# Performance work log

Measured on AMD Instinct MI355X. Metric: run time of the kernel, lower is better.

## Reference

```python
import jax, jax.numpy as jnp
import numpy as np

D_MODEL = 1024
NUM_HEADS = 16
SEQ_LEN = 2048
HEAD_DIM = D_MODEL // NUM_HEADS


def _rope_thetas(seq_len, head_dim):
    # Standard RoPE angles: theta[s, j] = s * 10000^(-2j/d), j in [0, d/2)
    d_half = head_dim // 2
    pos = jnp.arange(seq_len, dtype=jnp.float32)
    freqs = 1.0 / jnp.power(10000.0, jnp.arange(0, head_dim, 2, dtype=jnp.float32) / head_dim)
    thetas = pos[:, None] * freqs[None, :]  # [S, d_half]
    return jnp.cos(thetas), jnp.sin(thetas)


def _apply_rope(x, cos, sin):
    # x: [B, H, S, D]; rotate consecutive pairs (x_{2i}, x_{2i+1}) by theta_i
    b, h, s, d = x.shape
    xp = x.reshape(b, h, s, d // 2, 2)
    x1, x2 = xp[..., 0], xp[..., 1]
    c = cos[None, None, :, :]
    sn = sin[None, None, :, :]
    o1 = x1 * c - x2 * sn
    o2 = x1 * sn + x2 * c
    return jnp.stack([o1, o2], axis=-1).reshape(b, h, s, d)


def setup_inputs() -> dict:
    key = jax.random.key(0)
    k_x, k_wqkv, k_bqkv, k_wo, k_bo = jax.random.split(key, 5)
    lim_qkv = 1.0 / np.sqrt(D_MODEL)
    x = jax.random.normal(k_x, (2, SEQ_LEN, D_MODEL), dtype=jnp.float32)
    w_qkv = jax.random.uniform(k_wqkv, (3 * D_MODEL, D_MODEL), jnp.float32, -lim_qkv, lim_qkv)
    b_qkv = jax.random.uniform(k_bqkv, (3 * D_MODEL,), jnp.float32, -lim_qkv, lim_qkv)
    w_out = jax.random.uniform(k_wo, (D_MODEL, D_MODEL), jnp.float32, -lim_qkv, lim_qkv)
    b_out = jax.random.uniform(k_bo, (D_MODEL,), jnp.float32, -lim_qkv, lim_qkv)
    return {"x": x, "w_qkv": w_qkv, "b_qkv": b_qkv, "w_out": w_out, "b_out": b_out}


def reference(x, w_qkv, b_qkv, w_out, b_out):
    B, S, D = x.shape
    H, Dh = NUM_HEADS, D // NUM_HEADS
    qkv = x @ w_qkv.T + b_qkv  # [B, S, 3D]
    q, k, v = jnp.split(qkv, 3, axis=-1)
    # [B, S, D] -> [B, H, S, Dh]
    q = q.reshape(B, S, H, Dh).transpose(0, 2, 1, 3)
    k = k.reshape(B, S, H, Dh).transpose(0, 2, 1, 3)
    v = v.reshape(B, S, H, Dh).transpose(0, 2, 1, 3)
    cos, sin = _rope_thetas(S, Dh)
    q = _apply_rope(q, cos, sin)
    k = _apply_rope(k, cos, sin)
    scores = jnp.einsum('bhqd,bhkd->bhqk', q, k) / jnp.sqrt(jnp.float32(Dh))
    causal = jnp.tril(jnp.ones((S, S), dtype=bool))
    scores = jnp.where(causal[None, None, :, :], scores, jnp.float32(-jnp.inf))
    attn = jax.nn.softmax(scores, axis=-1)
    o = jnp.einsum('bhqk,bhkd->bhqd', attn, v)  # [B, H, S, Dh]
    o = o.transpose(0, 2, 1, 3).reshape(B, S, D)
    return o @ w_out.T + b_out
```

## Files before the change

### kernel.cpp

```cpp
#include <hip/hip_runtime.h>
#include <stdint.h>

#define S_LEN 2048
#define NH 16
#define DM 1024
#define HD 64
#define NB 2
#define TOK (NB * S_LEN)

typedef __attribute__((ext_vector_type(8))) short short8v;
typedef __attribute__((ext_vector_type(4))) float f32x4;
typedef __attribute__((ext_vector_type(2))) unsigned int u32x2;
typedef unsigned short u16;
typedef unsigned int u32;

__device__ __forceinline__ float bf2f(u16 u) {
    u32 x = ((u32)u) << 16;
    return __builtin_bit_cast(float, x);
}
__device__ __forceinline__ u16 f2bf(float f) {
    u32 u = __builtin_bit_cast(u32, f);
    return (u16)((u + 0x7FFFu + ((u >> 16) & 1u)) >> 16);
}
__device__ __forceinline__ u32 cvtpk(float lo, float hi) {
    u32 r;
    asm("v_cvt_pk_bf16_f32 %0, %1, %2" : "=v"(r) : "v"(lo), "v"(hi));
    return r;
}

__device__ __forceinline__ void gld_lds16(const void* g, void* lds_base_uniform) {
    auto gp = (const __attribute__((address_space(1))) u32*)(uintptr_t)g;
    auto lp = (__attribute__((address_space(3))) u32*)(uintptr_t)(u32)(uintptr_t)lds_base_uniform;
    __builtin_amdgcn_global_load_lds(gp, lp, 16, 0, 0);
}

__global__ void detect_dtype(const u32* __restrict__ xw, int* __restrict__ flag) {
    __shared__ int cnt[4];
    const int t = threadIdx.x;
    int c = 0;
#pragma unroll
    for (int j = 0; j < 16; ++j) {
        const u32 wd = xw[(t * 16 + j) * 64];
        const u32 e = (wd >> 7) & 0xFF;
        c += (e >= 0x58 && e <= 0x98) ? 1 : 0;
    }
#pragma unroll
    for (int off = 1; off < 64; off <<= 1) c += __shfl_xor(c, off);
    if ((t & 63) == 0) cnt[t >> 6] = c;
    __syncthreads();
    if (t == 0) flag[0] = (cnt[0] + cnt[1] + cnt[2] + cnt[3] >= 2600) ? 1 : 0;
}

#define XCH (TOK * DM / 8)
#define WQCH (3 * DM * DM / 8)
#define WOCH (DM * DM / 8)
#define CONVTOT (XCH + WQCH + WOCH)
#define TABN (S_LEN * 16)
__global__ __launch_bounds__(256) void convert_all(
    const void* __restrict__ xs, const void* __restrict__ wqs, const void* __restrict__ wos,
    u16* __restrict__ xd, u16* __restrict__ wqd, u16* __restrict__ wod,
    float* __restrict__ tab, const int* __restrict__ flagp) {
    int i = blockIdx.x * 256 + threadIdx.x;
    if (i >= CONVTOT) {
        const int e = i - CONVTOT;
        const int s = e & 2047;
        const int i2 = e >> 11;
        const float fa = expf(-(float)(2 * i2) * 0.2878231366242557f);
        const float fb = expf(-(float)(2 * i2 + 1) * 0.2878231366242557f);
        float sa, ca, sb, cb;
        sincosf((float)s * fa, &sa, &ca);
        sincosf((float)s * fb, &sb, &cb);
        f32x4 tv = {ca, sa, cb, sb};
        *(f32x4*)(tab + (size_t)e * 4) = tv;
        return;
    }
    const void* src;
    u16* dst;
    if (i < XCH) {
        src = xs; dst = xd;
    } else if (i < XCH + WQCH) {
        src = wqs; dst = wqd; i -= XCH;
    } else {
        src = wos; dst = wod; i -= XCH + WQCH;
    }
    if (flagp[0]) {
        ((short8v*)dst)[i] = ((const short8v*)src)[i];
    } else {
        const f32x4 v0 = ((const f32x4*)src)[2 * i];
        const f32x4 v1 = ((const f32x4*)src)[2 * i + 1];
        short8v o;
#pragma unroll
        for (int q = 0; q < 4; ++q) o[q] = (short)f2bf(v0[q]);
#pragma unroll
        for (int q = 0; q < 4; ++q) o[4 + q] = (short)f2bf(v1[q]);
        ((short8v*)dst)[i] = o;
    }
}

template <int MODE>
__global__ __launch_bounds__(256) void gemm_k(
    const u16* __restrict__ A, const u16* __restrict__ Bt,
    const void* __restrict__ biasv, void* __restrict__ Cv,
    int M, int N, int K, const int* __restrict__ flagp, int out_flagged,
    u16* __restrict__ qws, u16* __restrict__ kws,
    u16* __restrict__ vT, const float* __restrict__ tab) {
    __shared__ __align__(16) u16 lA[3][128 * 32];
    __shared__ __align__(16) u16 lB[3][128 * 32];
    const int fl = flagp[0];
    const int fo = out_flagged ? fl : 1;

    const int tid = threadIdx.x;
    const int w = __builtin_amdgcn_readfirstlane(tid >> 6);
    const int lane = tid & 63;
    const int quad = lane >> 4;
    const int l16 = lane & 15;
    const int bm = blockIdx.y * 128;
    const int bn = (MODE == 2 ? 2048 : 0) + blockIdx.x * 128;
    const int wm = (w >> 1) * 64;
    const int wn = (w & 1) * 64;

    f32x4 acc[4][4];
#pragma unroll
    for (int i = 0; i < 4; ++i)
#pragma unroll
        for (int j = 0; j < 4; ++j) acc[i][j] = {0.f, 0.f, 0.f, 0.f};

    const int kiters = K >> 5;
#define GEMM_STAGE(kk, buf)                                                            \
    {                                                                                  \
        _Pragma("unroll") for (int c = 0; c < 2; ++c) {                                \
            const int chunk = w * 2 + c;                                               \
            const int off = chunk * 1024 + lane * 16;                                  \
            const int m_ = off >> 6;                                                   \
            const int kb_ = off & 63;                                                  \
            gld_lds16((const char*)(A + (size_t)(bm + m_) * K + (kk) * 32) + kb_,      \
                      (char*)&lA[buf][0] + chunk * 1024);                              \
            gld_lds16((const char*)(Bt + (size_t)(bn + m_) * K + (kk) * 32) + kb_,     \
                      (char*)&lB[buf][0] + chunk * 1024);                              \
        }                                                                              \
    }

    GEMM_STAGE(0, 0);
    if (kiters > 1) GEMM_STAGE(1, 1);
    int cur = 0;
    for (int kk = 0; kk < kiters; ++kk) {
        if (kk + 1 < kiters) {
            asm volatile("s_waitcnt vmcnt(4)" ::: "memory");
        } else {
            asm volatile("s_waitcnt vmcnt(0)" ::: "memory");
        }
        __builtin_amdgcn_s_barrier();
        if (kk + 2 < kiters) {
            const int nb = (cur + 2 >= 3) ? cur - 1 : cur + 2;
            GEMM_STAGE(kk + 2, nb);
        }

        short8v af[4], bf[4];
#pragma unroll
        for (int t = 0; t < 4; ++t) {
            af[t] = *(const short8v*)&lA[cur][(wm + t * 16 + l16) * 32 + quad * 8];
            bf[t] = *(const short8v*)&lB[cur][(wn + t * 16 + l16) * 32 + quad * 8];
        }
        __builtin_amdgcn_s_setprio(1);
        if constexpr (MODE == 2) {
#pragma unroll
            for (int i = 0; i < 4; ++i)
#pragma unroll
                for (int j = 0; j < 4; ++j)
                    acc[i][j] =
                        __builtin_amdgcn_mfma_f32_16x16x32_bf16(af[i], bf[j], acc[i][j], 0, 0, 0);
        } else {
#pragma unroll
            for (int i = 0; i < 4; ++i)
#pragma unroll
                for (int j = 0; j < 4; ++j)
                    acc[i][j] =
                        __builtin_amdgcn_mfma_f32_16x16x32_bf16(bf[j], af[i], acc[i][j], 0, 0, 0);
        }
        __builtin_amdgcn_s_setprio(0);
        cur = (cur == 2) ? 0 : cur + 1;
    }
#undef GEMM_STAGE

    if constexpr (MODE == 0) {
#pragma unroll
        for (int j = 0; j < 4; ++j) {
            const int n0 = bn + wn + j * 16 + quad * 4;
            float bv0, bv1, bv2, bv3;
            if (fl) {
                const u32x2 bw = *(const u32x2*)((const u16*)biasv + n0);
                bv0 = bf2f((u16)(bw.x & 0xffff));
                bv1 = bf2f((u16)(bw.x >> 16));
                bv2 = bf2f((u16)(bw.y & 0xffff));
                bv3 = bf2f((u16)(bw.y >> 16));
            } else {
                const f32x4 bw = *(const f32x4*)((const float*)biasv + n0);
                bv0 = bw[0]; bv1 = bw[1]; bv2 = bw[2]; bv3 = bw[3];
            }
#pragma unroll
            for (int i = 0; i < 4; ++i) {
                const size_t base = (size_t)(bm + wm + i * 16 + l16) * N + n0;
                const float v0 = acc[i][j][0] + bv0, v1 = acc[i][j][1] + bv1;
                const float v2 = acc[i][j][2] + bv2, v3 = acc[i][j][3] + bv3;
                if (fo) {
                    u32x2 ov;
                    ov.x = cvtpk(v0, v1);
                    ov.y = cvtpk(v2, v3);
                    *(u32x2*)((u16*)Cv + base) = ov;
                } else {
                    f32x4 ov = {v0, v1, v2, v3};
                    *(f32x4*)((float*)Cv + base) = ov;
                }
            }
        }
    } else if constexpr (MODE == 2) {
#pragma unroll
        for (int j = 0; j < 4; ++j) {
            const int n = bn + wn + j * 16 + l16;
            const float bv = fl ? bf2f(((const u16*)biasv)[n]) : ((const float*)biasv)[n];
            const int vcol = n - 2048;
            const int hh = vcol >> 6, d = vcol & 63;
#pragma unroll
            for (int i = 0; i < 4; ++i) {
                const int m0 = bm + wm + i * 16 + quad * 4;
                const int bb = m0 >> 11, s0 = m0 & 2047;
                u32x2 ov;
                ov.x = cvtpk(acc[i][j][0] + bv, acc[i][j][1] + bv);
                ov.y = cvtpk(acc[i][j][2] + bv, acc[i][j][3] + bv);
                *(u32x2*)(vT + ((size_t)((bb * NH + hh) * HD + d)) * S_LEN + s0) = ov;
            }
        }
    } else {
        const bool isq = (blockIdx.x < 8);
        u16* outp = isq ? qws : kws;
#pragma unroll
        for (int j = 0; j < 4; ++j) {
            const int n0 = bn + wn + j * 16 + quad * 4;
            float bv0, bv1, bv2, bv3;
            if (fl) {
                const u32x2 bw = *(const u32x2*)((const u16*)biasv + n0);
                bv0 = bf2f((u16)(bw.x & 0xffff));
                bv1 = bf2f((u16)(bw.x >> 16));
                bv2 = bf2f((u16)(bw.y & 0xffff));
                bv3 = bf2f((u16)(bw.y >> 16));
            } else {
                const f32x4 bw = *(const f32x4*)((const float*)biasv + n0);
                bv0 = bw[0]; bv1 = bw[1]; bv2 = bw[2]; bv3 = bw[3];
            }
            const int nc = n0 & 1023;
            const int hh = nc >> 6;
            const int d0 = nc & 63;
            const int i2u = d0 >> 2;
#pragma unroll
            for (int i = 0; i < 4; ++i) {
                const int m = bm + wm + i * 16 + l16;
                const int bb = m >> 11, s = m & 2047;
                const f32x4 cs4 = *(const f32x4*)(tab + ((size_t)i2u * S_LEN + s) * 4);
                const float v0 = acc[i][j][0] + bv0, v1 = acc[i][j][1] + bv1;
                const float v2 = acc[i][j][2] + bv2, v3 = acc[i][j][3] + bv3;
                const float o0 = v0 * cs4[0] - v1 * cs4[1];
                const float o1 = v0 * cs4[1] + v1 * cs4[0];
                const float o2 = v2 * cs4[2] - v3 * cs4[3];
                const float o3 = v2 * cs4[3] + v3 * cs4[2];
                u32x2 ov;
                ov.x = cvtpk(o0, o1);
                ov.y = cvtpk(o2, o3);
                *(u32x2*)(outp + ((size_t)((bb * NH + hh) * S_LEN + s)) * HD + d0) = ov;
            }
        }
    }
}

__global__ __launch_bounds__(256, 3) void attn_kernel(
    const u16* __restrict__ qws, const u16* __restrict__ kws,
    const u16* __restrict__ vT, u16* __restrict__ ows) {
    __shared__ __align__(16) u16 kl[3][64 * 64];
    __shared__ __align__(16) u16 vl[2][64 * 64];
    __shared__ __align__(16) u32 pl32[4][16 * 36];
    const int t = threadIdx.x;
    const int w = __builtin_amdgcn_readfirstlane(t >> 6);
    const int lane = t & 63;
    const int quad = lane >> 4;
    const int l16 = lane & 15;

    const int id = blockIdx.x;
    const int g = id & 31;
    const int qb = 31 - (id >> 5);
    const int h = g & 15, b = g >> 4;
    const int q0 = qb * 64 + w * 16;

    const size_t bh = (size_t)(b * NH + h);
    const u16* qbp = qws + bh * (size_t)S_LEN * HD;
    const u16* kb = kws + bh * (size_t)S_LEN * HD;
    const u16* vb = vT + bh * (size_t)HD * S_LEN;

    const int r0 = lane >> 3;
    const int srcc = (lane & 7) ^ r0;
    const int xorb = (l16 & 7) << 4;

    short8v qf[2];
#pragma unroll
    for (int hf = 0; hf < 2; ++hf)
        qf[hf] = *(const short8v*)(qbp + (size_t)(q0 + l16) * HD + hf * 32 + quad * 8);

    f32x4 oaccT[4];
#pragma unroll
    for (int d = 0; d < 4; ++d) oaccT[d] = {0.f, 0.f, 0.f, 0.f};
    float mrow = -__builtin_inff();
    float lrow = 0.f;

#define STAGE_K(kt, buf)                                                            \
    {                                                                               \
        _Pragma("unroll") for (int s = 0; s < 2; ++s) {                             \
            const int row = w * 8 + s * 32 + r0;                                    \
            gld_lds16(kb + (size_t)((kt) * 64 + row) * HD + srcc * 8,               \
                      (char*)&kl[buf][0] + w * 1024 + s * 4096);                    \
        }                                                                           \
    }
#define STAGE_V(kt, buf)                                                            \
    {                                                                               \
        _Pragma("unroll") for (int s = 0; s < 2; ++s) {                             \
            const int row = w * 8 + s * 32 + r0;                                    \
            gld_lds16(vb + (size_t)row * S_LEN + (kt) * 64 + srcc * 8,              \
                      (char*)&vl[buf][0] + w * 1024 + s * 4096);                    \
        }                                                                           \
    }

    STAGE_K(0, 0);
    STAGE_V(0, 0);
    if (qb >= 1) STAGE_K(1, 1);

    int ck = 0;
    for (int kt = 0; kt <= qb; ++kt) {
        if (kt < qb) {
            asm volatile("s_waitcnt vmcnt(2)" ::: "memory");
        } else {
            asm volatile("s_waitcnt vmcnt(0)" ::: "memory");
        }
        __builtin_amdgcn_s_barrier();
        asm volatile("" ::: "memory");
        if (kt < qb) STAGE_V(kt + 1, (kt + 1) & 1);
        if (kt + 2 <= qb) {
            const int kn = (ck + 2 >= 3) ? ck - 1 : ck + 2;
            STAGE_K(kt + 2, kn);
        }
        const char* Kb = (const char*)&kl[ck][0];
        const char* Vb = (const char*)&vl[kt & 1][0];

        f32x4 s4[4];
        __builtin_amdgcn_s_setprio(1);
#pragma unroll
        for (int sub = 0; sub < 4; ++sub) {
            const int lin = (sub * 16 + l16) * 128 + quad * 16;
            const short8v k0 = *(const short8v*)(Kb + (lin ^ xorb));
            const short8v k1 = *(const short8v*)(Kb + ((lin + 64) ^ xorb));
            f32x4 a = {0.f, 0.f, 0.f, 0.f};
            a = __builtin_amdgcn_mfma_f32_16x16x32_bf16(k0, qf[0], a, 0, 0, 0);
            a = __builtin_amdgcn_mfma_f32_16x16x32_bf16(k1, qf[1], a, 0, 0, 0);
            s4[sub] = a;
        }
        __builtin_amdgcn_s_setprio(0);
        float sv[16];
#pragma unroll
        for (int sub = 0; sub < 4; ++sub)
#pragma unroll
            for (int r = 0; r < 4; ++r) sv[sub * 4 + r] = s4[sub][r] * 0.125f;
        if (kt == qb) {
            const int qloc = w * 16 + l16;
#pragma unroll
            for (int sub = 0; sub < 4; ++sub)
#pragma unroll
                for (int r = 0; r < 4; ++r)
                    if (sub * 16 + quad * 4 + r > qloc) sv[sub * 4 + r] = -__builtin_inff();
        }
        float a0 = fmaxf(sv[0], sv[1]), a1 = fmaxf(sv[2], sv[3]);
        float a2 = fmaxf(sv[4], sv[5]), a3 = fmaxf(sv[6], sv[7]);
        float a4 = fmaxf(sv[8], sv[9]), a5 = fmaxf(sv[10], sv[11]);
        float a6 = fmaxf(sv[12], sv[13]), a7 = fmaxf(sv[14], sv[15]);
        a0 = fmaxf(a0, a1); a2 = fmaxf(a2, a3);
        a4 = fmaxf(a4, a5); a6 = fmaxf(a6, a7);
        a0 = fmaxf(a0, a2); a4 = fmaxf(a4, a6);
        float mx = fmaxf(a0, a4);
        mx = fmaxf(mx, __shfl_xor(mx, 16));
        mx = fmaxf(mx, __shfl_xor(mx, 32));
        const float mnew = fmaxf(mrow, mx);
        const float alpha = __expf(mrow - mnew);
        mrow = mnew;
        float p[16];
#pragma unroll
        for (int i = 0; i < 16; ++i) p[i] = __expf(sv[i] - mnew);
        float b0 = p[0] + p[1], b1 = p[2] + p[3], b2 = p[4] + p[5], b3 = p[6] + p[7];
        float b4 = p[8] + p[9], b5 = p[10] + p[11], b6 = p[12] + p[13], b7 = p[14] + p[15];
        b0 += b1; b2 += b3; b4 += b5; b6 += b7;
        b0 += b2; b4 += b6;
        float ps = b0 + b4;
        ps += __shfl_xor(ps, 16);
        ps += __shfl_xor(ps, 32);
        lrow = lrow * alpha + ps;
#pragma unroll
        for (int d = 0; d < 4; ++d) oaccT[d] *= alpha;
        u32* prow = &pl32[w][l16 * 36];
#pragma unroll
        for (int sub = 0; sub < 4; ++sub) {
            u32x2 pw;
            pw.x = cvtpk(p[sub * 4 + 0], p[sub * 4 + 1]);
            pw.y = cvtpk(p[sub * 4 + 2], p[sub * 4 + 3]);
            *(u32x2*)&prow[sub * 8 + quad * 2] = pw;
        }
        asm volatile("s_waitcnt lgkmcnt(0)" ::: "memory");
        __builtin_amdgcn_sched_barrier(0);
        __builtin_amdgcn_s_setprio(1);
#pragma unroll
        for (int c2 = 0; c2 < 2; ++c2) {
            const short8v pf = *(const short8v*)&pl32[w][l16 * 36 + c2 * 16 + quad * 4];
#pragma unroll
            for (int d = 0; d < 4; ++d) {
                const int lin = (d * 16 + l16) * 128 + c2 * 64 + quad * 16;
                const short8v vfd = *(const short8v*)(Vb + (lin ^ xorb));
                oaccT[d] = __builtin_amdgcn_mfma_f32_16x16x32_bf16(vfd, pf, oaccT[d], 0, 0, 0);
            }
        }
        __builtin_amdgcn_s_setprio(0);
        ck = (ck == 2) ? 0 : ck + 1;
    }
#undef STAGE_K
#undef STAGE_V

    const float inv = 1.0f / lrow;
    const size_t rowbase = ((size_t)(b * S_LEN + q0 + l16)) * DM + h * HD;
#pragma unroll
    for (int df = 0; df < 4; ++df) {
        const int d0 = df * 16 + quad * 4;
        u32x2 ov;
        ov.x = cvtpk(oaccT[df][0] * inv, oaccT[df][1] * inv);
        ov.y = cvtpk(oaccT[df][2] * inv, oaccT[df][3] * inv);
        *(u32x2*)(ows + rowbase + d0) = ov;
    }
}

extern "C" void kernel_launch(void* const* d_in, const int* in_sizes, int n_in,
                              void* d_out, int out_size, void* d_ws, size_t ws_size,
                              hipStream_t stream) {
    const void* x = d_in[0];
    const void* w_qkv = d_in[1];
    const void* b_qkv = d_in[2];
    const void* w_out = d_in[3];
    const void* b_out = d_in[4];

    int* flag = (int*)d_ws;
    u16* xb = (u16*)d_ws + 8;
    u16* wqkvb = xb + (size_t)TOK * DM;
    u16* woutb = wqkvb + (size_t)3 * DM * DM;
    u16* qws = woutb + (size_t)DM * DM;
    u16* kws = qws + (size_t)NB * NH * S_LEN * HD;
    u16* vT = kws + (size_t)NB * NH * S_LEN * HD;
    u16* ows = vT + (size_t)NB * NH * HD * S_LEN;
    float* tab = (float*)(ows + (size_t)TOK * DM);

    detect_dtype<<<1, 256, 0, stream>>>((const u32*)x, flag);
    convert_all<<<(CONVTOT + TABN) / 256, 256, 0, stream>>>(
        x, w_qkv, w_out, xb, wqkvb, woutb, tab, flag);

    gemm_k<1><<<dim3(16, TOK / 128), 256, 0, stream>>>(
        xb, wqkvb, b_qkv, nullptr, TOK, 3 * DM, DM, flag, 0, qws, kws, nullptr, tab);
    gemm_k<2><<<dim3(8, TOK / 128), 256, 0, stream>>>(
        xb, wqkvb, b_qkv, nullptr, TOK, 3 * DM, DM, flag, 0, nullptr, nullptr, vT, nullptr);
    attn_kernel<<<dim3(32 * 32), 256, 0, stream>>>(qws, kws, vT, ows);
    gemm_k<0><<<dim3(DM / 128, TOK / 128), 256, 0, stream>>>(
        ows, woutb, b_out, d_out, TOK, DM, DM, flag, 1, nullptr, nullptr, nullptr, nullptr);
}
```

Baseline: 209.8 us.

## Process two query tiles per attention block to reuse K/V loads

Each attention block now handles two 64-row query tiles (rows qb*128.. and +64) against the same staged K/V tiles, halving the grid. This reuses every K/V LDS load for two Q tiles and reorders block indices to mix long and short causal rows. In exchange it drops the triple-buffered K prefetch for double buffering with a full vmcnt(0) wait each iteration, and it raises register pressure from the duplicated accumulators.

```diff
diff --git a/kernel.cpp b/kernel.cpp
--- a/kernel.cpp
+++ b/kernel.cpp
@@ -274,9 +274,9 @@
 __global__ __launch_bounds__(256, 3) void attn_kernel(
     const u16* __restrict__ qws, const u16* __restrict__ kws,
     const u16* __restrict__ vT, u16* __restrict__ ows) {
-    __shared__ __align__(16) u16 kl[3][64 * 64];
+    __shared__ __align__(16) u16 kl[2][64 * 64];
     __shared__ __align__(16) u16 vl[2][64 * 64];
-    __shared__ __align__(16) u32 pl32[4][16 * 36];
+    __shared__ __align__(16) u32 pl32[4][2][16 * 36];
     const int t = threadIdx.x;
     const int w = __builtin_amdgcn_readfirstlane(t >> 6);
     const int lane = t & 63;
@@ -285,9 +285,12 @@
 
     const int id = blockIdx.x;
     const int g = id & 31;
-    const int qb = 31 - (id >> 5);
+    const int qbr = id >> 5;
+    const int qb = (qbr < 8) ? (15 - qbr) : (qbr - 8);
     const int h = g & 15, b = g >> 4;
-    const int q0 = qb * 64 + w * 16;
+    const int qrow = qb * 128 + w * 16;
+    const int ktl0 = 2 * qb;
+    const int ktl1 = 2 * qb + 1;
 
     const size_t bh = (size_t)(b * NH + h);
     const u16* qbp = qws + bh * (size_t)S_LEN * HD;
@@ -298,16 +301,21 @@
     const int srcc = (lane & 7) ^ r0;
     const int xorb = (l16 & 7) << 4;
 
-    short8v qf[2];
-#pragma unroll
-    for (int hf = 0; hf < 2; ++hf)
-        qf[hf] = *(const short8v*)(qbp + (size_t)(q0 + l16) * HD + hf * 32 + quad * 8);
-
-    f32x4 oaccT[4];
-#pragma unroll
-    for (int d = 0; d < 4; ++d) oaccT[d] = {0.f, 0.f, 0.f, 0.f};
-    float mrow = -__builtin_inff();
-    float lrow = 0.f;
+    short8v qf0[2], qf1[2];
+#pragma unroll
+    for (int hf = 0; hf < 2; ++hf) {
+        qf0[hf] = *(const short8v*)(qbp + (size_t)(qrow + l16) * HD + hf * 32 + quad * 8);
+        qf1[hf] = *(const short8v*)(qbp + (size_t)(qrow + 64 + l16) * HD + hf * 32 + quad * 8);
+    }
+
+    f32x4 oacc0[4], oacc1[4];
+#pragma unroll
+    for (int d = 0; d < 4; ++d) {
+        oacc0[d] = {0.f, 0.f, 0.f, 0.f};
+        oacc1[d] = {0.f, 0.f, 0.f, 0.f};
+    }
+    float mrow0 = -__builtin_inff(), mrow1 = -__builtin_inff();
+    float lrow0 = 0.f, lrow1 = 0.f;
 
 #define STAGE_K(kt, buf)                                                            \
     {                                                                               \
@@ -326,28 +334,83 @@
         }                                                                           \
     }
 
+#define SMPV(hh, S, DIAG)                                                              \
+    {                                                                                  \
+        float sv[16];                                                                  \
+        _Pragma("unroll") for (int sub = 0; sub < 4; ++sub)                            \
+            _Pragma("unroll") for (int r = 0; r < 4; ++r)                              \
+                sv[sub * 4 + r] = S[sub][r] * 0.125f;                                  \
+        if (DIAG) {                                                                    \
+            const int qloc = w * 16 + l16;                                             \
+            _Pragma("unroll") for (int sub = 0; sub < 4; ++sub)                        \
+                _Pragma("unroll") for (int r = 0; r < 4; ++r)                          \
+                    if (sub * 16 + quad * 4 + r > qloc)                                \
+                        sv[sub * 4 + r] = -__builtin_inff();                           \
+        }                                                                              \
+        float a0 = fmaxf(sv[0], sv[1]), a1 = fmaxf(sv[2], sv[3]);                      \
+        float a2 = fmaxf(sv[4], sv[5]), a3 = fmaxf(sv[6], sv[7]);                      \
+        float a4 = fmaxf(sv[8], sv[9]), a5 = fmaxf(sv[10], sv[11]);                    \
+        float a6 = fmaxf(sv[12], sv[13]), a7 = fmaxf(sv[14], sv[15]);                  \
+        a0 = fmaxf(a0, a1); a2 = fmaxf(a2, a3);                                        \
+        a4 = fmaxf(a4, a5); a6 = fmaxf(a6, a7);                                        \
+        a0 = fmaxf(a0, a2); a4 = fmaxf(a4, a6);                                        \
+        float mx = fmaxf(a0, a4);                                                      \
+        mx = fmaxf(mx, __shfl_xor(mx, 16));                                            \
+        mx = fmaxf(mx, __shfl_xor(mx, 32));                                            \
+        const float mnew = fmaxf(mrow##hh, mx);                                        \
+        const float alpha = __expf(mrow##hh - mnew);                                   \
+        mrow##hh = mnew;                                                               \
+        float p[16];                                                                   \
+        _Pragma("unroll") for (int i = 0; i < 16; ++i) p[i] = __expf(sv[i] - mnew);    \
+        float c0 = p[0] + p[1], c1 = p[2] + p[3], c2_ = p[4] + p[5], c3 = p[6] + p[7]; \
+        float c4 = p[8] + p[9], c5 = p[10] + p[11], c6 = p[12] + p[13],                \
+              c7 = p[14] + p[15];                                                      \
+        c0 += c1; c2_ += c3; c4 += c5; c6 += c7;                                       \
+        c0 += c2_; c4 += c6;                                                           \
+        float ps = c0 + c4;                                                            \
+        ps += __shfl_xor(ps, 16);                                                      \
+        ps += __shfl_xor(ps, 32);                                                      \
+        lrow##hh = lrow##hh * alpha + ps;                                              \
+        _Pragma("unroll") for (int d = 0; d < 4; ++d) oacc##hh[d] *= alpha;            \
+        u32* prow = &pl32[w][hh][l16 * 36];                                            \
+        _Pragma("unroll") for (int sub = 0; sub < 4; ++sub) {                          \
+            u32x2 pw;                                                                  \
+            pw.x = cvtpk(p[sub * 4 + 0], p[sub * 4 + 1]);                              \
+            pw.y = cvtpk(p[sub * 4 + 2], p[sub * 4 + 3]);                              \
+            *(u32x2*)&prow[sub * 8 + quad * 2] = pw;                                   \
+        }                                                                              \
+        asm volatile("s_waitcnt lgkmcnt(0)" ::: "memory");                             \
+        __builtin_amdgcn_sched_barrier(0);                                             \
+        __builtin_amdgcn_s_setprio(1);                                                 \
+        _Pragma("unroll") for (int c2 = 0; c2 < 2; ++c2) {                             \
+            const short8v pf =                                                         \
+                *(const short8v*)&pl32[w][hh][l16 * 36 + c2 * 16 + quad * 4];          \
+            _Pragma("unroll") for (int d = 0; d < 4; ++d) {                            \
+                const int lin = (d * 16 + l16) * 128 + c2 * 64 + quad * 16;            \
+                const short8v vfd = *(const short8v*)(Vb + (lin ^ xorb));              \
+                oacc##hh[d] =                                                          \
+                    __builtin_amdgcn_mfma_f32_16x16x32_bf16(vfd, pf, oacc##hh[d], 0, 0, 0); \
+            }                                                                          \
+        }                                                                              \
+        __builtin_amdgcn_s_setprio(0);                                                 \
+    }
+
     STAGE_K(0, 0);
     STAGE_V(0, 0);
-    if (qb >= 1) STAGE_K(1, 1);
-
-    int ck = 0;
-    for (int kt = 0; kt <= qb; ++kt) {
-        if (kt < qb) {
-            asm volatile("s_waitcnt vmcnt(2)" ::: "memory");
-        } else {
-            asm volatile("s_waitcnt vmcnt(0)" ::: "memory");
-        }
+
+    for (int kt = 0; kt <= ktl1; ++kt) {
+        asm volatile("s_waitcnt vmcnt(0)" ::: "memory");
         __builtin_amdgcn_s_barrier();
         asm volatile("" ::: "memory");
-        if (kt < qb) STAGE_V(kt + 1, (kt + 1) & 1);
-        if (kt + 2 <= qb) {
-            const int kn = (ck + 2 >= 3) ? ck - 1 : ck + 2;
-            STAGE_K(kt + 2, kn);
-        }
-        const char* Kb = (const char*)&kl[ck][0];
+        if (kt < ktl1) {
+            STAGE_V(kt + 1, (kt + 1) & 1);
+            STAGE_K(kt + 1, (kt + 1) & 1);
+        }
+        const char* Kb = (const char*)&kl[kt & 1][0];
         const char* Vb = (const char*)&vl[kt & 1][0];
 
-        f32x4 s4[4];
+        const bool h0act = (kt <= ktl0);
+        f32x4 sA[4], sB[4];
         __builtin_amdgcn_s_setprio(1);
 #pragma unroll
         for (int sub = 0; sub < 4; ++sub) {
@@ -355,86 +418,48 @@
             const short8v k0 = *(const short8v*)(Kb + (lin ^ xorb));
             const short8v k1 = *(const short8v*)(Kb + ((lin + 64) ^ xorb));
             f32x4 a = {0.f, 0.f, 0.f, 0.f};
-            a = __builtin_amdgcn_mfma_f32_16x16x32_bf16(k0, qf[0], a, 0, 0, 0);
-            a = __builtin_amdgcn_mfma_f32_16x16x32_bf16(k1, qf[1], a, 0, 0, 0);
-            s4[sub] = a;
+            if (h0act) {
+                a = __builtin_amdgcn_mfma_f32_16x16x32_bf16(k0, qf0[0], a, 0, 0, 0);
+                a = __builtin_amdgcn_mfma_f32_16x16x32_bf16(k1, qf0[1], a, 0, 0, 0);
+            }
+            sA[sub] = a;
+            f32x4 bq = {0.f, 0.f, 0.f, 0.f};
+            bq = __builtin_amdgcn_mfma_f32_16x16x32_bf16(k0, qf1[0], bq, 0, 0, 0);
+            bq = __builtin_amdgcn_mfma_f32_16x16x32_bf16(k1, qf1[1], bq, 0, 0, 0);
+            sB[sub] = bq;
         }
         __builtin_amdgcn_s_setprio(0);
-        float sv[16];
-#pragma unroll
-        for (int sub = 0; sub < 4; ++sub)
-#pragma unroll
-            for (int r = 0; r < 4; ++r) sv[sub * 4 + r] = s4[sub][r] * 0.125f;
-        if (kt == qb) {
-            const int qloc = w * 16 + l16;
-#pragma unroll
-            for (int sub = 0; sub < 4; ++sub)
-#pragma unroll
-                for (int r = 0; r < 4; ++r)
-                    if (sub * 16 + quad * 4 + r > qloc) sv[sub * 4 + r] = -__builtin_inff();
-        }
-        float a0 = fmaxf(sv[0], sv[1]), a1 = fmaxf(sv[2], sv[3]);
-        float a2 = fmaxf(sv[4], sv[5]), a3 = fmaxf(sv[6], sv[7]);
-        float a4 = fmaxf(sv[8], sv[9]), a5 = fmaxf(sv[10], sv[11]);
-        float a6 = fmaxf(sv[12], sv[13]), a7 = fmaxf(sv[14], sv[15]);
-        a0 = fmaxf(a0, a1); a2 = fmaxf(a2, a3);
-        a4 = fmaxf(a4, a5); a6 = fmaxf(a6, a7);
-        a0 = fmaxf(a0, a2); a4 = fmaxf(a4, a6);
-        float mx = fmaxf(a0, a4);
-        mx = fmaxf(mx, __shfl_xor(mx, 16));
-        mx = fmaxf(mx, __shfl_xor(mx, 32));
-        const float mnew = fmaxf(mrow, mx);
-        const float alpha = __expf(mrow - mnew);
-        mrow = mnew;
-        float p[16];
-#pragma unroll
-        for (int i = 0; i < 16; ++i) p[i] = __expf(sv[i] - mnew);
-        float b0 = p[0] + p[1], b1 = p[2] + p[3], b2 = p[4] + p[5], b3 = p[6] + p[7];
-        float b4 = p[8] + p[9], b5 = p[10] + p[11], b6 = p[12] + p[13], b7 = p[14] + p[15];
-        b0 += b1; b2 += b3; b4 += b5; b6 += b7;
-        b0 += b2; b4 += b6;
-        float ps = b0 + b4;
-        ps += __shfl_xor(ps, 16);
-        ps += __shfl_xor(ps, 32);
-        lrow = lrow * alpha + ps;
-#pragma unroll
-        for (int d = 0; d < 4; ++d) oaccT[d] *= alpha;
-        u32* prow = &pl32[w][l16 * 36];
-#pragma unroll
-        for (int sub = 0; sub < 4; ++sub) {
-            u32x2 pw;
-            pw.x = cvtpk(p[sub * 4 + 0], p[sub * 4 + 1]);
-            pw.y = cvtpk(p[sub * 4 + 2], p[sub * 4 + 3]);
-            *(u32x2*)&prow[sub * 8 + quad * 2] = pw;
-        }
-        asm volatile("s_waitcnt lgkmcnt(0)" ::: "memory");
-        __builtin_amdgcn_sched_barrier(0);
-        __builtin_amdgcn_s_setprio(1);
-#pragma unroll
-        for (int c2 = 0; c2 < 2; ++c2) {
-            const short8v pf = *(const short8v*)&pl32[w][l16 * 36 + c2 * 16 + quad * 4];
-#pragma unroll
-            for (int d = 0; d < 4; ++d) {
-                const int lin = (d * 16 + l16) * 128 + c2 * 64 + quad * 16;
-                const short8v vfd = *(const short8v*)(Vb + (lin ^ xorb));
-                oaccT[d] = __builtin_amdgcn_mfma_f32_16x16x32_bf16(vfd, pf, oaccT[d], 0, 0, 0);
-            }
-        }
-        __builtin_amdgcn_s_setprio(0);
-        ck = (ck == 2) ? 0 : ck + 1;
+
+        if (h0act) SMPV(0, sA, kt == ktl0);
+        SMPV(1, sB, kt == ktl1);
     }
 #undef STAGE_K
 #undef STAGE_V
-
-    const float inv = 1.0f / lrow;
-    const size_t rowbase = ((size_t)(b * S_LEN + q0 + l16)) * DM + h * HD;
-#pragma unroll
-    for (int df = 0; df < 4; ++df) {
-        const int d0 = df * 16 + quad * 4;
-        u32x2 ov;
-        ov.x = cvtpk(oaccT[df][0] * inv, oaccT[df][1] * inv);
-        ov.y = cvtpk(oaccT[df][2] * inv, oaccT[df][3] * inv);
-        *(u32x2*)(ows + rowbase + d0) = ov;
+#undef SMPV
+
+    {
+        const float inv = 1.0f / lrow0;
+        const size_t rowbase = ((size_t)(b * S_LEN + qrow + l16)) * DM + h * HD;
+#pragma unroll
+        for (int df = 0; df < 4; ++df) {
+            const int d0 = df * 16 + quad * 4;
+            u32x2 ov;
+            ov.x = cvtpk(oacc0[df][0] * inv, oacc0[df][1] * inv);
+            ov.y = cvtpk(oacc0[df][2] * inv, oacc0[df][3] * inv);
+            *(u32x2*)(ows + rowbase + d0) = ov;
+        }
+    }
+    {
+        const float inv = 1.0f / lrow1;
+        const size_t rowbase = ((size_t)(b * S_LEN + qrow + 64 + l16)) * DM + h * HD;
+#pragma unroll
+        for (int df = 0; df < 4; ++df) {
+            const int d0 = df * 16 + quad * 4;
+            u32x2 ov;
+            ov.x = cvtpk(oacc1[df][0] * inv, oacc1[df][1] * inv);
+            ov.y = cvtpk(oacc1[df][2] * inv, oacc1[df][3] * inv);
+            *(u32x2*)(ows + rowbase + d0) = ov;
+        }
     }
 }
 
@@ -465,7 +490,7 @@
         xb, wqkvb, b_qkv, nullptr, TOK, 3 * DM, DM, flag, 0, qws, kws, nullptr, tab);
     gemm_k<2><<<dim3(8, TOK / 128), 256, 0, stream>>>(
         xb, wqkvb, b_qkv, nullptr, TOK, 3 * DM, DM, flag, 0, nullptr, nullptr, vT, nullptr);
-    attn_kernel<<<dim3(32 * 32), 256, 0, stream>>>(qws, kws, vT, ows);
+    attn_kernel<<<dim3(16 * 32), 256, 0, stream>>>(qws, kws, vT, ows);
     gemm_k<0><<<dim3(DM / 128, TOK / 128), 256, 0, stream>>>(
         ows, woutb, b_out, d_out, TOK, DM, DM, flag, 1, nullptr, nullptr, nullptr, nullptr);
 }
```

Measured after the change: 221.7 us. +5.7%, slower.
